# Performance work log

Hardware: AMD Instinct MI355X
Metric: run time of the kernel (lower is better)

Reference implementation:

```python
import jax, jax.numpy as jnp
import numpy as np

N_NODES = 50000
N_EDGES = 800000
IN_SIZE = 128
HID = 128
OUT_SIZE = 64
N_LAYERS = 2
MAXK = 32


def setup_inputs() -> dict:
    key = jax.random.key(0)
    ks = jax.random.split(key, 8)
    s = 0.05  # small init scale, xavier-like
    return {
        "x": jax.random.normal(ks[0], (N_NODES, IN_SIZE), dtype=jnp.float32),
        "W_in": jax.random.normal(ks[1], (IN_SIZE, HID), dtype=jnp.float32) * s,
        "b_in": jnp.zeros((HID,), dtype=jnp.float32),
        "W_self": jax.random.normal(ks[2], (N_LAYERS, HID, HID), dtype=jnp.float32) * s,
        "W_neigh": jax.random.normal(ks[3], (N_LAYERS, HID, HID), dtype=jnp.float32) * s,
        "W_out": jax.random.normal(ks[4], (HID, OUT_SIZE), dtype=jnp.float32) * s,
        "b_out": jnp.zeros((OUT_SIZE,), dtype=jnp.float32),
        "edge_index": jax.random.randint(ks[5], (2, N_EDGES), 0, N_NODES, dtype=jnp.int32),
        "k": MAXK,
    }


def _maxk(x, k):
    # Keep top-k values per row, zero out the rest (MaxK nonlinearity).
    vals, idx = jax.lax.top_k(x, k)                     # [N, k]
    rows = jnp.arange(x.shape[0])[:, None]
    return jnp.zeros_like(x).at[rows, idx].set(vals)


def reference(x, W_in, b_in, W_self, W_neigh, W_out, b_out, edge_index, k):
    N = x.shape[0]
    src, dst = edge_index[0], edge_index[1]
    # Row sums of the (src->dst) adjacency = out-degree of src, per original code.
    deg = jax.ops.segment_sum(jnp.ones((src.shape[0],), dtype=x.dtype), src,
                              num_segments=N)[:, None]  # [N, 1]
    h = x @ W_in + b_in                                  # lin_in
    for i in range(W_self.shape[0]):
        hs = _maxk(h, k)                                 # MaxK sparsify [N, H]
        # adj @ hs : out[i] = sum over edges (i -> j) of hs[j]; then mean-normalize
        agg = jax.ops.segment_sum(hs[dst], src, num_segments=N) / (deg + 1e-6)
        h = hs @ W_self[i] + agg @ W_neigh[i]            # h_self + h_neigh
        # dropout (eval) and Identity norm are no-ops
    return h @ W_out + b_out                             # lin_out
```

## Files before the change

kernel.cpp:

```cpp
#include <hip/hip_runtime.h>

#define KDIM 128
#define NNODE 50000
#define CHSTRIDE 800000

typedef _Float16 f16x8 __attribute__((ext_vector_type(8)));
typedef _Float16 f16x4 __attribute__((ext_vector_type(4)));
typedef float f32x16 __attribute__((ext_vector_type(16)));

#define NRANGE 6250
#define ECHUNK 3200

__global__ void hist_kernel(const int* __restrict__ src, int* __restrict__ cnt, int E) {
    const int r = blockIdx.x & 7;
    const int chunk = blockIdx.x >> 3;
    const int lo = r * NRANGE, hi = lo + NRANGE;
    const int base = chunk * ECHUNK;
    const int end = min(base + ECHUNK, E);
    for (int i = base + threadIdx.x; i < end; i += 256) {
        int s = src[i];
        if (s >= lo && s < hi) atomicAdd(&cnt[s], 1);
    }
}

__global__ void scatter_kernel(const int* __restrict__ src, const int* __restrict__ dst,
                               int* cursor, int* __restrict__ col, int E) {
    const int r = blockIdx.x & 7;
    const int chunk = blockIdx.x >> 3;
    const int lo = r * NRANGE, hi = lo + NRANGE;
    const int base = chunk * ECHUNK;
    const int end = min(base + ECHUNK, E);
    for (int i = base + threadIdx.x; i < end; i += 256) {
        int s = src[i];
        if (s >= lo && s < hi) {
            int p = atomicAdd(&cursor[s], 1);
            col[p] = dst[i];
        }
    }
}

__global__ void scan1_kernel(const int* __restrict__ cnt, int* __restrict__ row_ptr,
                             int* __restrict__ bsum, int N) {
    __shared__ int ws[4];
    const int t = threadIdx.x;
    const int lane = t & 63, w = t >> 6;
    const int i = blockIdx.x * 256 + t;
    int v = (i < N) ? cnt[i] : 0;
    int x = v;
    #pragma unroll
    for (int off = 1; off < 64; off <<= 1) {
        int u = __shfl_up(x, off);
        if (lane >= off) x += u;
    }
    if (lane == 63) ws[w] = x;
    __syncthreads();
    int wexcl = 0;
    #pragma unroll
    for (int k = 0; k < 4; k++) wexcl += (k < w) ? ws[k] : 0;
    if (i < N) row_ptr[i] = wexcl + x - v;
    if (t == 255) bsum[blockIdx.x] = wexcl + x;
}

__global__ void scan2_kernel(int* __restrict__ bsum, int NB) {
    __shared__ int ws[4];
    const int t = threadIdx.x;
    const int lane = t & 63, w = t >> 6;
    int v = (t < NB) ? bsum[t] : 0;
    int x = v;
    #pragma unroll
    for (int off = 1; off < 64; off <<= 1) {
        int u = __shfl_up(x, off);
        if (lane >= off) x += u;
    }
    if (lane == 63) ws[w] = x;
    __syncthreads();
    int wexcl = 0;
    #pragma unroll
    for (int k = 0; k < 4; k++) wexcl += (k < w) ? ws[k] : 0;
    if (t < NB) bsum[t] = wexcl + x - v;
}

__global__ void scan3_kernel(const int* __restrict__ bsum, int* __restrict__ row_ptr,
                             int* __restrict__ cursor, int N, int E) {
    const int i = blockIdx.x * 256 + threadIdx.x;
    if (i < N) {
        int v = row_ptr[i] + bsum[blockIdx.x];
        row_ptr[i] = v;
        cursor[i] = v;
    }
    if (i == 0) row_ptr[N] = E;
}

__global__ void sortrows_kernel(const int* __restrict__ row_ptr, int* __restrict__ col, int M) {
    int wid = (blockIdx.x * blockDim.x + threadIdx.x) >> 6;
    int lane = threadIdx.x & 63;
    if (wid >= M) return;
    int s = row_ptr[wid], e = row_ptr[wid + 1], len = e - s;
    if (len <= 1) return;
    if (len <= 64) {
        int v = (lane < len) ? col[s + lane] : 0x7fffffff;
        #pragma unroll
        for (int k = 2; k <= 64; k <<= 1) {
            #pragma unroll
            for (int j = k >> 1; j > 0; j >>= 1) {
                int o = __shfl_xor(v, j);
                bool dir = ((lane & k) == 0);
                bool smaller = ((lane & j) == 0);
                int mn = min(v, o), mx = max(v, o);
                v = (dir == smaller) ? mn : mx;
            }
        }
        if (lane < len) col[s + lane] = v;
    } else if (lane == 0) {
        for (int a = s + 1; a < e; a++) {
            int key = col[a];
            int b = a - 1;
            while (b >= s && col[b] > key) { col[b + 1] = col[b]; b--; }
            col[b + 1] = key;
        }
    }
}

__global__ void maxk_kernel(const float* __restrict__ h, float* __restrict__ hsc, int M) {
    int wid = (blockIdx.x * blockDim.x + threadIdx.x) >> 6;
    int lane = threadIdx.x & 63;
    if (wid >= M) return;
    float2 v = ((const float2*)(h + (size_t)wid * KDIM))[lane];

    unsigned int u0 = __float_as_uint(v.x);
    u0 = (u0 & 0x80000000u) ? ~u0 : (u0 | 0x80000000u);
    unsigned int u1 = __float_as_uint(v.y);
    u1 = (u1 & 0x80000000u) ? ~u1 : (u1 | 0x80000000u);

    unsigned int prefix = 0;
    int remaining = 32;
    #pragma unroll
    for (int b = 31; b >= 0; --b) {
        unsigned int candHi = (prefix >> b) | 1u;
        unsigned long long m0 = __ballot((u0 >> b) == candHi);
        unsigned long long m1 = __ballot((u1 >> b) == candHi);
        int cnt = __popcll(m0) + __popcll(m1);
        if (cnt >= remaining) prefix |= (1u << b);
        else remaining -= cnt;
    }

    unsigned long long e0 = __ballot(u0 == prefix);
    unsigned long long e1 = __ballot(u1 == prefix);
    unsigned long long g0 = __ballot(u0 > prefix);
    unsigned long long g1 = __ballot(u1 > prefix);
    int quota = 32 - (__popcll(g0) + __popcll(g1));
    unsigned long long below = (1ULL << lane) - 1ULL;
    int rank0 = __popcll(e0 & below) + __popcll(e1 & below);
    int rank1 = rank0 + (int)((e0 >> lane) & 1ULL);
    bool k0 = (u0 > prefix) || (((e0 >> lane) & 1ULL) && rank0 < quota);
    bool k1 = (u1 > prefix) || (((e1 >> lane) & 1ULL) && rank1 < quota);

    float2 o;
    o.x = k0 ? v.x : 0.0f;
    o.y = k1 ? v.y : 0.0f;
    ((float2*)(hsc + (size_t)(lane >> 3) * CHSTRIDE))[(size_t)wid * 8 + (lane & 7)] = o;
}

#define ANPB 16
#define AECAP 1024

__global__ __launch_bounds__(256)
void aggregate_kernel(const float* __restrict__ hsc, const int* __restrict__ row_ptr,
                      const int* __restrict__ col, float* __restrict__ agg, int M) {
    __shared__ int cols[AECAP];
    const int c = blockIdx.x & 7;
    const int g = blockIdx.x >> 3;
    const int n0 = g * ANPB;
    const int tid = threadIdx.x;
    const int w = tid >> 6;
    const int lane = tid & 63;
    const int ng = lane >> 4;
    const int e2 = (lane >> 3) & 1;
    const int f2 = lane & 7;

    const int nend = min(n0 + ANPB, M);
    const int base0 = row_ptr[n0];
    const int ecount = row_ptr[nend] - base0;
    const bool fits = (ecount <= AECAP);
    if (fits) {
        for (int i = tid; i < ecount; i += 256) cols[i] = col[base0 + i];
    }
    __syncthreads();

    const int n = n0 + w * 4 + ng;
    const bool valid = (n < M);
    const int s = valid ? (row_ptr[n] - base0) : 0;
    const int e = valid ? (row_ptr[n + 1] - base0) : 0;
    const char* bp = (const char*)(hsc + (size_t)c * CHSTRIDE) + f2 * 8;

    float ax = 0.f, ay = 0.f, bx = 0.f, by = 0.f;
    int j = s + e2;
    if (fits) {
        for (; j + 2 < e; j += 4) {
            unsigned o0 = (unsigned)cols[j] << 6;
            unsigned o1 = (unsigned)cols[j + 2] << 6;
            float2 v0 = *(const float2*)(bp + o0);
            float2 v1 = *(const float2*)(bp + o1);
            ax += v0.x; ay += v0.y;
            bx += v1.x; by += v1.y;
        }
        if (j < e) {
            float2 v = *(const float2*)(bp + ((unsigned)cols[j] << 6));
            ax += v.x; ay += v.y;
        }
    } else {
        const int* cg = col + base0;
        for (; j + 2 < e; j += 4) {
            unsigned o0 = (unsigned)cg[j] << 6;
            unsigned o1 = (unsigned)cg[j + 2] << 6;
            float2 v0 = *(const float2*)(bp + o0);
            float2 v1 = *(const float2*)(bp + o1);
            ax += v0.x; ay += v0.y;
            bx += v1.x; by += v1.y;
        }
        if (j < e) {
            float2 v = *(const float2*)(bp + ((unsigned)cg[j] << 6));
            ax += v.x; ay += v.y;
        }
    }

    float tx = ax + bx, ty = ay + by;
    tx += __shfl_xor(tx, 8);
    ty += __shfl_xor(ty, 8);
    if (valid && e2 == 0) {
        float inv = 1.0f / ((float)(e - s) + 1e-6f);
        float2 o;
        o.x = tx * inv;
        o.y = ty * inv;
        ((float2*)(agg + (size_t)n * KDIM + c * 16))[f2] = o;
    }
}

__global__ void conv_wt_kernel(const float* __restrict__ W_in,
                               const float* __restrict__ W_self,
                               const float* __restrict__ W_neigh,
                               const float* __restrict__ W_out,
                               _Float16* __restrict__ wb) {
    int t = blockIdx.x * blockDim.x + threadIdx.x;
    if (t < 81920) {
        int m = t >> 14;
        int e = t & 16383;
        int n = e >> 7, k = e & 127;
        const float* S = (m == 0) ? W_in
                       : (m <= 2) ? (W_self + (size_t)(m - 1) * 16384)
                                  : (W_neigh + (size_t)(m - 3) * 16384);
        float v = S[k * 128 + n];
        _Float16 hi = (_Float16)v;
        _Float16 lo = (_Float16)(v - (float)hi);
        int pair = m * 2;
        wb[(size_t)pair * 16384 + n * 128 + k] = hi;
        wb[(size_t)(pair + 1) * 16384 + n * 128 + k] = lo;
    } else if (t < 90112) {
        int e = t - 81920;
        int n = e >> 7, k = e & 127;
        float v = W_out[k * 64 + n];
        _Float16 hi = (_Float16)v;
        _Float16 lo = (_Float16)(v - (float)hi);
        wb[(size_t)10 * 16384 + e] = hi;
        wb[(size_t)11 * 16384 + e] = lo;
    }
}

template <int BN, bool DUAL, bool BIAS, bool A1CHUNK>
__global__ __launch_bounds__(256)
void gemm_mfma(const float* __restrict__ A1, const float* __restrict__ A2,
               const _Float16* __restrict__ B1h, const _Float16* __restrict__ B1l,
               const _Float16* __restrict__ B2h, const _Float16* __restrict__ B2l,
               const float* __restrict__ bias, float* __restrict__ C, int M) {
    constexpr int NSRC = DUAL ? 2 : 1;
    constexpr int NT = BN / 32;
    constexpr int TPW = NT / 2;

    __shared__ __align__(16) char Alds[2 * 64 * 256];

    const int tid = threadIdx.x;
    const int w = tid >> 6;
    const int lane = tid & 63;
    const int l31 = lane & 31;
    const int kslot = lane >> 5;
    const int row0 = blockIdx.x * 64;

    const int n0 = (BN == 128) ? w * 32 : (w & 1) * 32;
    const int mt0 = (BN == 128) ? 0 : (w >> 1);

    f32x16 acc[TPW];
    #pragma unroll
    for (int t = 0; t < TPW; t++)
        #pragma unroll
        for (int e = 0; e < 16; e++) acc[t][e] = 0.0f;

    for (int s = 0; s < NSRC; s++) {
        if (s) __syncthreads();
        const float* A = s ? A2 : A1;
        #pragma unroll
        for (int p = 0; p < 8; p++) {
            int idx = tid + p * 256;
            int row = idx >> 5, k4 = idx & 31;
            float4 v = make_float4(0.f, 0.f, 0.f, 0.f);
            if (row0 + row < M) {
                if (A1CHUNK && s == 0)
                    v = *(const float4*)(A + (size_t)(k4 >> 2) * CHSTRIDE
                                           + (size_t)(row0 + row) * 16 + (k4 & 3) * 4);
                else
                    v = *(const float4*)(A + (size_t)(row0 + row) * KDIM + k4 * 4);
            }
            _Float16 h0 = (_Float16)v.x, h1 = (_Float16)v.y,
                     h2 = (_Float16)v.z, h3 = (_Float16)v.w;
            f16x4 hv = {h0, h1, h2, h3};
            f16x4 lv = {(_Float16)(v.x - (float)h0), (_Float16)(v.y - (float)h1),
                        (_Float16)(v.z - (float)h2), (_Float16)(v.w - (float)h3)};
            int boff = (k4 * 8) ^ ((row & 7) << 4);
            *(f16x4*)(Alds + row * 256 + boff) = hv;
            *(f16x4*)(Alds + 16384 + row * 256 + boff) = lv;
        }
        __syncthreads();

        const _Float16* Bh = s ? B2h : B1h;
        const _Float16* Bl = s ? B2l : B1l;
        const _Float16* bph = Bh + (size_t)(n0 + l31) * 128 + kslot * 8;
        const _Float16* bpl = Bl + (size_t)(n0 + l31) * 128 + kslot * 8;
        #pragma unroll
        for (int kb = 0; kb < 8; kb++) {
            f16x8 bh = *(const f16x8*)(bph + kb * 16);
            f16x8 bl = *(const f16x8*)(bpl + kb * 16);
            #pragma unroll
            for (int t = 0; t < TPW; t++) {
                int row = (mt0 + t) * 32 + l31;
                int boff = ((kb * 2 + kslot) * 16) ^ ((row & 7) << 4);
                const char* rp = Alds + row * 256 + boff;
                f16x8 ah = *(const f16x8*)(rp);
                f16x8 al = *(const f16x8*)(rp + 16384);
                acc[t] = __builtin_amdgcn_mfma_f32_32x32x16_f16(al, bh, acc[t], 0, 0, 0);
                acc[t] = __builtin_amdgcn_mfma_f32_32x32x16_f16(ah, bl, acc[t], 0, 0, 0);
                acc[t] = __builtin_amdgcn_mfma_f32_32x32x16_f16(ah, bh, acc[t], 0, 0, 0);
            }
        }
    }

    float bv = 0.0f;
    if (BIAS) bv = bias[n0 + l31];
    #pragma unroll
    for (int t = 0; t < TPW; t++) {
        #pragma unroll
        for (int r = 0; r < 16; r++) {
            int row = row0 + (mt0 + t) * 32 + (r & 3) + 8 * (r >> 2) + 4 * kslot;
            if (row < M) C[(size_t)row * BN + n0 + l31] = acc[t][r] + bv;
        }
    }
}

extern "C" void kernel_launch(void* const* d_in, const int* in_sizes, int n_in,
                              void* d_out, int out_size, void* d_ws, size_t ws_size,
                              hipStream_t stream) {
    const float* x       = (const float*)d_in[0];
    const float* W_in    = (const float*)d_in[1];
    const float* b_in    = (const float*)d_in[2];
    const float* W_self  = (const float*)d_in[3];
    const float* W_neigh = (const float*)d_in[4];
    const float* W_out   = (const float*)d_in[5];
    const float* b_out   = (const float*)d_in[6];
    const int*   eidx    = (const int*)d_in[7];

    const int N = NNODE, E = 800000;
    const int* src = eidx;
    const int* dst = eidx + E;

    char* ws = (char*)d_ws;
    float* h   = (float*)(ws);
    float* hsc = (float*)(ws + 25600000);
    float* agg = (float*)(ws + 51200000);
    int* cnt     = (int*)(ws + 76800000);
    int* row_ptr = (int*)(ws + 77000000);
    int* cursor  = (int*)(ws + 77200016);
    int* col     = (int*)(ws + 77400016);
    _Float16* wb = (_Float16*)(ws + 80600016);
    int* bsum    = (int*)(ws + 81000016);

    const _Float16* WinT_h  = wb + (size_t)0 * 16384;
    const _Float16* WinT_l  = wb + (size_t)1 * 16384;
    const _Float16* WoutT_h = wb + (size_t)10 * 16384;
    const _Float16* WoutT_l = wb + (size_t)11 * 16384;

    const int NB = (N + 255) / 256;
    const int EG = ((E + ECHUNK - 1) / ECHUNK) * 8;
    const int AG = ((N + ANPB - 1) / ANPB) * 8;

    hipMemsetAsync(cnt, 0, N * sizeof(int), stream);
    hist_kernel<<<EG, 256, 0, stream>>>(src, cnt, E);
    scan1_kernel<<<NB, 256, 0, stream>>>(cnt, row_ptr, bsum, N);
    scan2_kernel<<<1, 256, 0, stream>>>(bsum, NB);
    scan3_kernel<<<NB, 256, 0, stream>>>(bsum, row_ptr, cursor, N, E);
    scatter_kernel<<<EG, 256, 0, stream>>>(src, dst, cursor, col, E);
    sortrows_kernel<<<(N + 3) / 4, 256, 0, stream>>>(row_ptr, col, N);
    conv_wt_kernel<<<(90112 + 255) / 256, 256, 0, stream>>>(W_in, W_self, W_neigh, W_out, wb);

    const int G = (N + 63) / 64;

    gemm_mfma<128, false, true, false><<<G, 256, 0, stream>>>(
        x, nullptr, WinT_h, WinT_l, nullptr, nullptr, b_in, h, N);

    for (int i = 0; i < 2; i++) {
        maxk_kernel<<<(N + 3) / 4, 256, 0, stream>>>(h, hsc, N);
        aggregate_kernel<<<AG, 256, 0, stream>>>(hsc, row_ptr, col, agg, N);
        const _Float16* WsT_h = wb + (size_t)(2 + 2 * i) * 16384;
        const _Float16* WsT_l = wb + (size_t)(3 + 2 * i) * 16384;
        const _Float16* WnT_h = wb + (size_t)(6 + 2 * i) * 16384;
        const _Float16* WnT_l = wb + (size_t)(7 + 2 * i) * 16384;
        gemm_mfma<128, true, false, true><<<G, 256, 0, stream>>>(
            hsc, agg, WsT_h, WsT_l, WnT_h, WnT_l, nullptr, h, N);
    }

    gemm_mfma<64, false, true, false><<<G, 256, 0, stream>>>(
        h, nullptr, WoutT_h, WoutT_l, nullptr, nullptr, b_out, (float*)d_out, N);
}
```

Before: 368.9 us.

## Fuse MaxK top-k sparsification into GEMM epilogue and prefetch second A operand

```diff
diff --git a/kernel.cpp b/kernel.cpp
--- a/kernel.cpp
+++ b/kernel.cpp
@@ -121,12 +121,7 @@
     }
 }
 
-__global__ void maxk_kernel(const float* __restrict__ h, float* __restrict__ hsc, int M) {
-    int wid = (blockIdx.x * blockDim.x + threadIdx.x) >> 6;
-    int lane = threadIdx.x & 63;
-    if (wid >= M) return;
-    float2 v = ((const float2*)(h + (size_t)wid * KDIM))[lane];
-
+__device__ __forceinline__ float2 maxk_row(float2 v, int lane) {
     unsigned int u0 = __float_as_uint(v.x);
     u0 = (u0 & 0x80000000u) ? ~u0 : (u0 | 0x80000000u);
     unsigned int u1 = __float_as_uint(v.y);
@@ -158,7 +153,7 @@
     float2 o;
     o.x = k0 ? v.x : 0.0f;
     o.y = k1 ? v.y : 0.0f;
-    ((float2*)(hsc + (size_t)(lane >> 3) * CHSTRIDE))[(size_t)wid * 8 + (lane & 7)] = o;
+    return o;
 }
 
 #define ANPB 16
@@ -266,12 +261,13 @@
     }
 }
 
-template <int BN, bool DUAL, bool BIAS, bool A1CHUNK>
+template <int BN, bool DUAL, bool BIAS, bool A1CHUNK, bool FUSE_MAXK>
 __global__ __launch_bounds__(256)
 void gemm_mfma(const float* __restrict__ A1, const float* __restrict__ A2,
                const _Float16* __restrict__ B1h, const _Float16* __restrict__ B1l,
                const _Float16* __restrict__ B2h, const _Float16* __restrict__ B2l,
-               const float* __restrict__ bias, float* __restrict__ C, int M) {
+               const float* __restrict__ bias, float* __restrict__ C,
+               float* __restrict__ hsc_out, int M) {
     constexpr int NSRC = DUAL ? 2 : 1;
     constexpr int NT = BN / 32;
     constexpr int TPW = NT / 2;
@@ -288,27 +284,37 @@
     const int n0 = (BN == 128) ? w * 32 : (w & 1) * 32;
     const int mt0 = (BN == 128) ? 0 : (w >> 1);
 
+    const int srow = tid >> 5;
+    const int k4 = tid & 31;
+
     f32x16 acc[TPW];
     #pragma unroll
     for (int t = 0; t < TPW; t++)
         #pragma unroll
         for (int e = 0; e < 16; e++) acc[t][e] = 0.0f;
 
+    float4 pa[8];
+    #pragma unroll
+    for (int p = 0; p < 8; p++) {
+        int row = srow + p * 8;
+        float4 v = make_float4(0.f, 0.f, 0.f, 0.f);
+        if (row0 + row < M) {
+            if (A1CHUNK)
+                v = *(const float4*)(A1 + (size_t)(k4 >> 2) * CHSTRIDE
+                                        + (size_t)(row0 + row) * 16 + (k4 & 3) * 4);
+            else
+                v = *(const float4*)(A1 + (size_t)(row0 + row) * KDIM + k4 * 4);
+        }
+        pa[p] = v;
+    }
+
+    #pragma unroll
     for (int s = 0; s < NSRC; s++) {
         if (s) __syncthreads();
-        const float* A = s ? A2 : A1;
         #pragma unroll
         for (int p = 0; p < 8; p++) {
-            int idx = tid + p * 256;
-            int row = idx >> 5, k4 = idx & 31;
-            float4 v = make_float4(0.f, 0.f, 0.f, 0.f);
-            if (row0 + row < M) {
-                if (A1CHUNK && s == 0)
-                    v = *(const float4*)(A + (size_t)(k4 >> 2) * CHSTRIDE
-                                           + (size_t)(row0 + row) * 16 + (k4 & 3) * 4);
-                else
-                    v = *(const float4*)(A + (size_t)(row0 + row) * KDIM + k4 * 4);
-            }
+            int row = srow + p * 8;
+            float4 v = pa[p];
             _Float16 h0 = (_Float16)v.x, h1 = (_Float16)v.y,
                      h2 = (_Float16)v.z, h3 = (_Float16)v.w;
             f16x4 hv = {h0, h1, h2, h3};
@@ -319,6 +325,17 @@
             *(f16x4*)(Alds + 16384 + row * 256 + boff) = lv;
         }
         __syncthreads();
+
+        if (s + 1 < NSRC) {
+            #pragma unroll
+            for (int p = 0; p < 8; p++) {
+                int row = srow + p * 8;
+                float4 v = make_float4(0.f, 0.f, 0.f, 0.f);
+                if (row0 + row < M)
+                    v = *(const float4*)(A2 + (size_t)(row0 + row) * KDIM + k4 * 4);
+                pa[p] = v;
+            }
+        }
 
         const _Float16* Bh = s ? B2h : B1h;
         const _Float16* Bl = s ? B2l : B1l;
@@ -344,12 +361,37 @@
 
     float bv = 0.0f;
     if (BIAS) bv = bias[n0 + l31];
-    #pragma unroll
-    for (int t = 0; t < TPW; t++) {
-        #pragma unroll
-        for (int r = 0; r < 16; r++) {
-            int row = row0 + (mt0 + t) * 32 + (r & 3) + 8 * (r >> 2) + 4 * kslot;
-            if (row < M) C[(size_t)row * BN + n0 + l31] = acc[t][r] + bv;
+
+    if constexpr (FUSE_MAXK) {
+        __syncthreads();
+        float* ht = (float*)Alds;
+        #pragma unroll
+        for (int t = 0; t < TPW; t++) {
+            #pragma unroll
+            for (int r = 0; r < 16; r++) {
+                int row = (mt0 + t) * 32 + (r & 3) + 8 * (r >> 2) + 4 * kslot;
+                ht[row * 128 + n0 + l31] = acc[t][r] + bv;
+            }
+        }
+        __syncthreads();
+        float* slab = hsc_out + (size_t)(lane >> 3) * CHSTRIDE;
+        #pragma unroll 1
+        for (int rr = 0; rr < 16; rr++) {
+            int row = w * 16 + rr;
+            float2 v = *(const float2*)(ht + row * 128 + lane * 2);
+            float2 o = maxk_row(v, lane);
+            int n = row0 + row;
+            if (n < M)
+                ((float2*)slab)[(size_t)n * 8 + (lane & 7)] = o;
+        }
+    } else {
+        #pragma unroll
+        for (int t = 0; t < TPW; t++) {
+            #pragma unroll
+            for (int r = 0; r < 16; r++) {
+                int row = row0 + (mt0 + t) * 32 + (r & 3) + 8 * (r >> 2) + 4 * kslot;
+                if (row < M) C[(size_t)row * BN + n0 + l31] = acc[t][r] + bv;
+            }
         }
     }
 }
@@ -371,9 +413,9 @@
     const int* dst = eidx + E;
 
     char* ws = (char*)d_ws;
-    float* h   = (float*)(ws);
-    float* hsc = (float*)(ws + 25600000);
-    float* agg = (float*)(ws + 51200000);
+    float* slabA = (float*)(ws);
+    float* slabB = (float*)(ws + 25600000);
+    float* agg   = (float*)(ws + 51200000);
     int* cnt     = (int*)(ws + 76800000);
     int* row_ptr = (int*)(ws + 77000000);
     int* cursor  = (int*)(ws + 77200016);
@@ -389,6 +431,7 @@
     const int NB = (N + 255) / 256;
     const int EG = ((E + ECHUNK - 1) / ECHUNK) * 8;
     const int AG = ((N + ANPB - 1) / ANPB) * 8;
+    const int G  = (N + 63) / 64;
 
     hipMemsetAsync(cnt, 0, N * sizeof(int), stream);
     hist_kernel<<<EG, 256, 0, stream>>>(src, cnt, E);
@@ -399,22 +442,19 @@
     sortrows_kernel<<<(N + 3) / 4, 256, 0, stream>>>(row_ptr, col, N);
     conv_wt_kernel<<<(90112 + 255) / 256, 256, 0, stream>>>(W_in, W_self, W_neigh, W_out, wb);
 
-    const int G = (N + 63) / 64;
-
-    gemm_mfma<128, false, true, false><<<G, 256, 0, stream>>>(
-        x, nullptr, WinT_h, WinT_l, nullptr, nullptr, b_in, h, N);
-
-    for (int i = 0; i < 2; i++) {
-        maxk_kernel<<<(N + 3) / 4, 256, 0, stream>>>(h, hsc, N);
-        aggregate_kernel<<<AG, 256, 0, stream>>>(hsc, row_ptr, col, agg, N);
-        const _Float16* WsT_h = wb + (size_t)(2 + 2 * i) * 16384;
-        const _Float16* WsT_l = wb + (size_t)(3 + 2 * i) * 16384;
-        const _Float16* WnT_h = wb + (size_t)(6 + 2 * i) * 16384;
-        const _Float16* WnT_l = wb + (size_t)(7 + 2 * i) * 16384;
-        gemm_mfma<128, true, false, true><<<G, 256, 0, stream>>>(
-            hsc, agg, WsT_h, WsT_l, WnT_h, WnT_l, nullptr, h, N);
-    }
-
-    gemm_mfma<64, false, true, false><<<G, 256, 0, stream>>>(
-        h, nullptr, WoutT_h, WoutT_l, nullptr, nullptr, b_out, (float*)d_out, N);
-}
+    gemm_mfma<128, false, true, false, true><<<G, 256, 0, stream>>>(
+        x, nullptr, WinT_h, WinT_l, nullptr, nullptr, b_in, nullptr, slabA, N);
+
+    aggregate_kernel<<<AG, 256, 0, stream>>>(slabA, row_ptr, col, agg, N);
+    gemm_mfma<128, true, false, true, true><<<G, 256, 0, stream>>>(
+        slabA, agg, wb + (size_t)2 * 16384, wb + (size_t)3 * 16384,
+        wb + (size_t)6 * 16384, wb + (size_t)7 * 16384, nullptr, nullptr, slabB, N);
+
+    aggregate_kernel<<<AG, 256, 0, stream>>>(slabB, row_ptr, col, agg, N);
+    gemm_mfma<128, true, false, true, false><<<G, 256, 0, stream>>>(
+        slabB, agg, wb + (size_t)4 * 16384, wb + (size_t)5 * 16384,
+        wb + (size_t)8 * 16384, wb + (size_t)9 * 16384, nullptr, slabA, nullptr, N);
+
+    gemm_mfma<64, false, true, false, false><<<G, 256, 0, stream>>>(
+        slabA, nullptr, WoutT_h, WoutT_l, nullptr, nullptr, b_out, (float*)d_out, nullptr, N);
+}
```

Measured after the change: 381.2 us. +3.3%, slower.
